# Kernel tuning notes

Hardware: AMD Instinct MI355X
Metric: run time of the kernel (lower is better)

The kernel has to match this reference:

```python
import jax, jax.numpy as jnp
import numpy as np

N_NODES = 100000
N_EDGES = 1600000
DIMS = [21, 32, 64, 128, 21]  # conv1..conv4 (conv4 in-dim fixed to 128; source's 100 is a bug)


def _glorot(key, fan_in, fan_out):
    s = jnp.sqrt(6.0 / (fan_in + fan_out))
    return jax.random.uniform(key, (fan_in, fan_out), jnp.float32, -s, s)


def setup_inputs() -> dict:
    key = jax.random.key(0)
    ks = jax.random.split(key, 6)
    x = jax.random.normal(ks[0], (N_NODES, DIMS[0]), jnp.float32)
    edge_index = jax.random.randint(ks[1], (2, N_EDGES), 0, N_NODES, jnp.int64)
    inp = {"x": x, "edge_index": edge_index}
    wkeys = jax.random.split(ks[2], 4)
    for i in range(4):
        inp[f"W{i+1}"] = _glorot(wkeys[i], DIMS[i], DIMS[i + 1])
        inp[f"b{i+1}"] = jnp.zeros((DIMS[i + 1],), jnp.float32)
    return inp


def gcn_conv(x, row, col, W, b):
    # PyG GCNConv: h = x W; symmetric normalization with self loops; aggregate; + bias
    N = x.shape[0]
    h = x @ W  # [N, F]
    deg = jnp.zeros((N,), h.dtype).at[col].add(1.0) + 1.0  # +1 for self loop
    dinv = jax.lax.rsqrt(deg)
    norm = dinv[row] * dinv[col]  # [E]
    agg = jnp.zeros_like(h).at[col].add(norm[:, None] * h[row])  # scatter messages
    agg = agg + (dinv * dinv)[:, None] * h  # self-loop contribution
    return agg + b


def reference(x, edge_index, W1, b1, W2, b2, W3, b3, W4, b4):
    row, col = edge_index[0], edge_index[1]
    x = jax.nn.relu(gcn_conv(x, row, col, W1, b1))
    x = jax.nn.relu(gcn_conv(x, row, col, W2, b2))
    x = jax.nn.relu(gcn_conv(x, row, col, W3, b3))
    x = gcn_conv(x, row, col, W4, b4)
    return x
```

## Files before the change

kernel.cpp:

```cpp
#include <hip/hip_runtime.h>

#define NN 100000
#define NE 1600000
#define SH 7
#define NB_BKT 782
#define BCAP 3072
#define CSRCAP 3200
#define CHUNK 8192
#define TILES_TOTAL 3125
#define PIPE_BLOCKS 512

static inline int cdiv(long long a, int b) { return (int)((a + b - 1) / b); }

__global__ void partition_kernel(const int* __restrict__ row, const int* __restrict__ col,
                                 int* __restrict__ bcur,
                                 unsigned int* __restrict__ packed, int E) {
    __shared__ int lh[NB_BKT];
    __shared__ int lbase[NB_BKT];
    for (int i = threadIdx.x; i < NB_BKT; i += 256) lh[i] = 0;
    __syncthreads();
    int base = blockIdx.x * CHUNK;
    int end = min(base + CHUNK, E);
    for (int e = base + threadIdx.x; e < end; e += 256) atomicAdd(&lh[col[e] >> SH], 1);
    __syncthreads();
    for (int i = threadIdx.x; i < NB_BKT; i += 256) {
        int v = lh[i];
        lbase[i] = v ? atomicAdd(&bcur[i], v) : 0;
        lh[i] = 0;
    }
    __syncthreads();
    for (int e = base + threadIdx.x; e < end; e += 256) {
        int c = col[e];
        int r = row[e];
        int b = c >> SH;
        int off = atomicAdd(&lh[b], 1);
        packed[lbase[b] + off] = ((unsigned)r << 7) | (unsigned)(c & 127);
    }
}

__global__ void bucket_nodes_place(const unsigned int* __restrict__ packed,
                                   const int* __restrict__ bcur, int* __restrict__ rowptr,
                                   int* __restrict__ rowend, float* __restrict__ dinv,
                                   int* __restrict__ csr_row, int N) {
    int b = blockIdx.x;
    __shared__ int lcnt[128];
    __shared__ int lcur[128];
    __shared__ int wt4[4];
    int t = threadIdx.x;
    if (t < 128) lcnt[t] = 0;
    __syncthreads();
    int s = b * BCAP;
    int e = bcur[b];
    for (int i = s + t; i < e; i += 256)
        atomicAdd(&lcnt[packed[i] & 127u], 1);
    __syncthreads();
    int node = (b << SH) + t;
    int v = (t < 128 && node < N) ? lcnt[t] + 1 : 0;
    int lane = t & 63, w = t >> 6;
    int incl = v;
#pragma unroll
    for (int off = 1; off < 64; off <<= 1) {
        int u = __shfl_up(incl, off, 64);
        if (lane >= off) incl += u;
    }
    if (lane == 63) wt4[w] = incl;
    __syncthreads();
    int woff = 0;
    for (int i = 0; i < w; i++) woff += wt4[i];
    int excl = woff + incl - v;
    if (t < 128 && node < N) {
        int start = b * CSRCAP + excl;
        rowptr[node] = start;
        rowend[node] = start + v;
        csr_row[start] = node;
        dinv[node] = rsqrtf((float)v);
        lcur[t] = start + 1;
    }
    __syncthreads();
    for (int i = s + t; i < e; i += 256) {
        unsigned p = packed[i];
        int r = (int)(p >> 7);
        int pos = atomicAdd(&lcur[p & 127u], 1);
        csr_row[pos] = r;
    }
}

__global__ void padx_kernel(const float* __restrict__ x, float* __restrict__ xp,
                            int* __restrict__ bcur, int N) {
    int idx = blockIdx.x * blockDim.x + threadIdx.x;
    if (idx < NB_BKT) bcur[idx] = idx * BCAP;
    if (idx >= N * 32) return;
    int n = idx >> 5;
    int k = idx & 31;
    xp[idx] = (k < 21) ? x[n * 21 + k] : 0.f;
}

template <int LPN, int FIN, int FOUT, int RJ, int OSTRIDE>
__global__ __launch_bounds__(512) void gather_gemm(
    const float4* __restrict__ h, const int* __restrict__ rowptr,
    const int* __restrict__ rowend, const int* __restrict__ csr_row,
    const float* __restrict__ dinv, const float* __restrict__ W,
    const float* __restrict__ b, float* __restrict__ out, int N) {
    constexpr int NT = 512 / LPN;
    constexpr int FINP = 4 * LPN;
    constexpr int XLD = FINP + 1;
    constexpr int JG = FOUT / RJ;
    __shared__ float xs[NT * XLD];
    __shared__ float Ws[FIN * FOUT];
    __shared__ float bs[FOUT];
    const int t = threadIdx.x;

    for (int i = t; i < FIN * FOUT; i += 512) Ws[i] = W[i];
    if (t < FOUT) bs[t] = b[t];

    const int l = t % LPN;
    const int ny = t / LPN;
    const int node = blockIdx.x * NT + ny;
    float4 acc = make_float4(0.f, 0.f, 0.f, 0.f);
    if (node < N) {
        int s = rowptr[node], e = rowend[node];
        float dn = dinv[node];
        int i = s;
        for (; i + 3 < e; i += 4) {
            int r0 = csr_row[i], r1 = csr_row[i + 1], r2 = csr_row[i + 2], r3 = csr_row[i + 3];
            float w0 = dinv[r0] * dn, w1 = dinv[r1] * dn, w2 = dinv[r2] * dn, w3 = dinv[r3] * dn;
            float4 a0 = h[(size_t)r0 * LPN + l];
            float4 a1 = h[(size_t)r1 * LPN + l];
            float4 a2 = h[(size_t)r2 * LPN + l];
            float4 a3 = h[(size_t)r3 * LPN + l];
            acc.x = fmaf(w0, a0.x, acc.x); acc.y = fmaf(w0, a0.y, acc.y);
            acc.z = fmaf(w0, a0.z, acc.z); acc.w = fmaf(w0, a0.w, acc.w);
            acc.x = fmaf(w1, a1.x, acc.x); acc.y = fmaf(w1, a1.y, acc.y);
            acc.z = fmaf(w1, a1.z, acc.z); acc.w = fmaf(w1, a1.w, acc.w);
            acc.x = fmaf(w2, a2.x, acc.x); acc.y = fmaf(w2, a2.y, acc.y);
            acc.z = fmaf(w2, a2.z, acc.z); acc.w = fmaf(w2, a2.w, acc.w);
            acc.x = fmaf(w3, a3.x, acc.x); acc.y = fmaf(w3, a3.y, acc.y);
            acc.z = fmaf(w3, a3.z, acc.z); acc.w = fmaf(w3, a3.w, acc.w);
        }
        for (; i < e; i++) {
            int r0 = csr_row[i];
            float w0 = dinv[r0] * dn;
            float4 a0 = h[(size_t)r0 * LPN + l];
            acc.x = fmaf(w0, a0.x, acc.x); acc.y = fmaf(w0, a0.y, acc.y);
            acc.z = fmaf(w0, a0.z, acc.z); acc.w = fmaf(w0, a0.w, acc.w);
        }
    }
    xs[ny * XLD + 4 * l + 0] = acc.x;
    xs[ny * XLD + 4 * l + 1] = acc.y;
    xs[ny * XLD + 4 * l + 2] = acc.z;
    xs[ny * XLD + 4 * l + 3] = acc.w;
    __syncthreads();

    const int jg = t % JG;
    const int ng = t / JG;
    float r[RJ];
#pragma unroll
    for (int jj = 0; jj < RJ; jj++) r[jj] = 0.f;
#pragma unroll 4
    for (int k = 0; k < FIN; k++) {
        float xv = xs[ng * XLD + k];
#pragma unroll
        for (int jj = 0; jj < RJ; jj++)
            r[jj] = fmaf(xv, Ws[k * FOUT + jg * RJ + jj], r[jj]);
    }
    int onode = blockIdx.x * NT + ng;
    if (onode < N) {
        float* orow = out + (size_t)onode * OSTRIDE + jg * RJ;
#pragma unroll
        for (int jj = 0; jj < RJ; jj++) r[jj] = fmaxf(r[jj] + bs[jg * RJ + jj], 0.f);
#pragma unroll
        for (int c = 0; c < RJ / 4; c++)
            *(float4*)&orow[4 * c] = make_float4(r[4 * c], r[4 * c + 1], r[4 * c + 2], r[4 * c + 3]);
    }
}

template <int LPN, bool BIAS, bool STORE21>
__global__ void gather4_kernel(const float4* __restrict__ h, const int* __restrict__ rowptr,
                               const int* __restrict__ rowend, const int* __restrict__ csr_row,
                               const float* __restrict__ dinv, const float* __restrict__ bias,
                               float* __restrict__ outp, int N) {
    int node = blockIdx.x * blockDim.y + threadIdx.y;
    if (node >= N) return;
    int l = threadIdx.x;
    int s = rowptr[node], e = rowend[node];
    float dn = dinv[node];
    float4 acc = make_float4(0.f, 0.f, 0.f, 0.f);
    int i = s;
    for (; i + 3 < e; i += 4) {
        int r0 = csr_row[i], r1 = csr_row[i + 1], r2 = csr_row[i + 2], r3 = csr_row[i + 3];
        float w0 = dinv[r0] * dn, w1 = dinv[r1] * dn, w2 = dinv[r2] * dn, w3 = dinv[r3] * dn;
        float4 a0 = h[(size_t)r0 * LPN + l];
        float4 a1 = h[(size_t)r1 * LPN + l];
        float4 a2 = h[(size_t)r2 * LPN + l];
        float4 a3 = h[(size_t)r3 * LPN + l];
        acc.x = fmaf(w0, a0.x, acc.x); acc.y = fmaf(w0, a0.y, acc.y);
        acc.z = fmaf(w0, a0.z, acc.z); acc.w = fmaf(w0, a0.w, acc.w);
        acc.x = fmaf(w1, a1.x, acc.x); acc.y = fmaf(w1, a1.y, acc.y);
        acc.z = fmaf(w1, a1.z, acc.z); acc.w = fmaf(w1, a1.w, acc.w);
        acc.x = fmaf(w2, a2.x, acc.x); acc.y = fmaf(w2, a2.y, acc.y);
        acc.z = fmaf(w2, a2.z, acc.z); acc.w = fmaf(w2, a2.w, acc.w);
        acc.x = fmaf(w3, a3.x, acc.x); acc.y = fmaf(w3, a3.y, acc.y);
        acc.z = fmaf(w3, a3.z, acc.z); acc.w = fmaf(w3, a3.w, acc.w);
    }
    for (; i < e; i++) {
        int r0 = csr_row[i];
        float w0 = dinv[r0] * dn;
        float4 a0 = h[(size_t)r0 * LPN + l];
        acc.x = fmaf(w0, a0.x, acc.x); acc.y = fmaf(w0, a0.y, acc.y);
        acc.z = fmaf(w0, a0.z, acc.z); acc.w = fmaf(w0, a0.w, acc.w);
    }
    if (STORE21) {
        int j = 4 * l;
        float v[4] = {acc.x, acc.y, acc.z, acc.w};
#pragma unroll
        for (int c = 0; c < 4; c++) {
            int jj = j + c;
            if (jj < 21) outp[(size_t)node * 21 + jj] = v[c] + (BIAS ? bias[jj] : 0.f);
        }
    } else {
        ((float4*)outp)[(size_t)node * LPN + l] = acc;
    }
}

__global__ __launch_bounds__(512, 4) void gather_gemm_l3l4_pipe(
    const float4* __restrict__ h, const int* __restrict__ rowptr,
    const int* __restrict__ rowend, const int* __restrict__ csr_row,
    const float* __restrict__ dinv, const float* __restrict__ W3,
    const float* __restrict__ b3, const float* __restrict__ W4,
    float* __restrict__ out, int N) {
    __shared__ float xs[2][32 * 65];
    __shared__ float4 W3v[64 * 32];
    __shared__ float4 W4v[16 * 48];
    __shared__ float b3s[128];
    const int t = threadIdx.x;
    const int b = blockIdx.x;

    for (int d = t; d < 64 * 32; d += 512) {
        int k = d >> 5;
        int jg = d & 7;
        int c = (d >> 3) & 3;
        W3v[d] = ((const float4*)W3)[(k << 5) + (jg << 2) + c];
    }
    for (int cid = t; cid < 16 * 48; cid += 512) {
        int i = cid / 48, rem = cid - i * 48;
        int jq = rem >> 3, jg = rem & 7;
        int k = jg * 16 + i;
        float v0 = (4 * jq + 0 < 21) ? W4[k * 21 + 4 * jq + 0] : 0.f;
        float v1 = (4 * jq + 1 < 21) ? W4[k * 21 + 4 * jq + 1] : 0.f;
        float v2 = (4 * jq + 2 < 21) ? W4[k * 21 + 4 * jq + 2] : 0.f;
        float v3 = (4 * jq + 3 < 21) ? W4[k * 21 + 4 * jq + 3] : 0.f;
        W4v[cid] = make_float4(v0, v1, v2, v3);
    }
    if (t < 128) b3s[t] = b3[t];
    __syncthreads();

    const int R = (TILES_TOTAL - b + PIPE_BLOCKS - 1) / PIPE_BLOCKS;

    for (int r = 0; r <= R; r++) {
        if (t < 256) {
            if (r < R) {
                const int l = t & 7;
                const int ny = t >> 3;
                const int node = (b + PIPE_BLOCKS * r) * 32 + ny;
                float4 acc0 = make_float4(0.f, 0.f, 0.f, 0.f);
                float4 acc1 = make_float4(0.f, 0.f, 0.f, 0.f);
                if (node < N) {
                    int s = rowptr[node], e = rowend[node];
                    float dn = dinv[node];
                    int i = s;
                    for (; i + 3 < e; i += 4) {
                        int r0 = csr_row[i], r1 = csr_row[i + 1];
                        int r2 = csr_row[i + 2], r3 = csr_row[i + 3];
                        float w0 = dinv[r0] * dn, w1 = dinv[r1] * dn;
                        float w2 = dinv[r2] * dn, w3 = dinv[r3] * dn;
                        const float4* p0 = h + (size_t)r0 * 16 + 2 * l;
                        const float4* p1 = h + (size_t)r1 * 16 + 2 * l;
                        const float4* p2 = h + (size_t)r2 * 16 + 2 * l;
                        const float4* p3 = h + (size_t)r3 * 16 + 2 * l;
                        float4 a0 = p0[0], c0 = p0[1];
                        float4 a1 = p1[0], c1 = p1[1];
                        float4 a2 = p2[0], c2 = p2[1];
                        float4 a3 = p3[0], c3 = p3[1];
                        acc0.x = fmaf(w0, a0.x, acc0.x); acc0.y = fmaf(w0, a0.y, acc0.y);
                        acc0.z = fmaf(w0, a0.z, acc0.z); acc0.w = fmaf(w0, a0.w, acc0.w);
                        acc1.x = fmaf(w0, c0.x, acc1.x); acc1.y = fmaf(w0, c0.y, acc1.y);
                        acc1.z = fmaf(w0, c0.z, acc1.z); acc1.w = fmaf(w0, c0.w, acc1.w);
                        acc0.x = fmaf(w1, a1.x, acc0.x); acc0.y = fmaf(w1, a1.y, acc0.y);
                        acc0.z = fmaf(w1, a1.z, acc0.z); acc0.w = fmaf(w1, a1.w, acc0.w);
                        acc1.x = fmaf(w1, c1.x, acc1.x); acc1.y = fmaf(w1, c1.y, acc1.y);
                        acc1.z = fmaf(w1, c1.z, acc1.z); acc1.w = fmaf(w1, c1.w, acc1.w);
                        acc0.x = fmaf(w2, a2.x, acc0.x); acc0.y = fmaf(w2, a2.y, acc0.y);
                        acc0.z = fmaf(w2, a2.z, acc0.z); acc0.w = fmaf(w2, a2.w, acc0.w);
                        acc1.x = fmaf(w2, c2.x, acc1.x); acc1.y = fmaf(w2, c2.y, acc1.y);
                        acc1.z = fmaf(w2, c2.z, acc1.z); acc1.w = fmaf(w2, c2.w, acc1.w);
                        acc0.x = fmaf(w3, a3.x, acc0.x); acc0.y = fmaf(w3, a3.y, acc0.y);
                        acc0.z = fmaf(w3, a3.z, acc0.z); acc0.w = fmaf(w3, a3.w, acc0.w);
                        acc1.x = fmaf(w3, c3.x, acc1.x); acc1.y = fmaf(w3, c3.y, acc1.y);
                        acc1.z = fmaf(w3, c3.z, acc1.z); acc1.w = fmaf(w3, c3.w, acc1.w);
                    }
                    for (; i < e; i++) {
                        int r0 = csr_row[i];
                        float w0 = dinv[r0] * dn;
                        const float4* p0 = h + (size_t)r0 * 16 + 2 * l;
                        float4 a0 = p0[0], c0 = p0[1];
                        acc0.x = fmaf(w0, a0.x, acc0.x); acc0.y = fmaf(w0, a0.y, acc0.y);
                        acc0.z = fmaf(w0, a0.z, acc0.z); acc0.w = fmaf(w0, a0.w, acc0.w);
                        acc1.x = fmaf(w0, c0.x, acc1.x); acc1.y = fmaf(w0, c0.y, acc1.y);
                        acc1.z = fmaf(w0, c0.z, acc1.z); acc1.w = fmaf(w0, c0.w, acc1.w);
                    }
                }
                float* xr = xs[r & 1] + ny * 65 + 8 * l;
                xr[0] = acc0.x; xr[1] = acc0.y; xr[2] = acc0.z; xr[3] = acc0.w;
                xr[4] = acc1.x; xr[5] = acc1.y; xr[6] = acc1.z; xr[7] = acc1.w;
            }
        } else {
            if (r >= 1) {
                const int jg = t & 7;
                const int ng = (t >> 3) & 31;
                const int node = (b + PIPE_BLOCKS * (r - 1)) * 32 + ng;
                const float* arow = xs[(r - 1) & 1] + ng * 65;

                float accA[16];
#pragma unroll
                for (int jj = 0; jj < 16; jj++) accA[jj] = 0.f;
#pragma unroll 4
                for (int k = 0; k < 64; k++) {
                    float xa = arow[k];
                    const float4* wb = &W3v[(k << 5) + jg];
#pragma unroll
                    for (int c = 0; c < 4; c++) {
                        float4 w = wb[c << 3];
                        accA[4 * c + 0] = fmaf(xa, w.x, accA[4 * c + 0]);
                        accA[4 * c + 1] = fmaf(xa, w.y, accA[4 * c + 1]);
                        accA[4 * c + 2] = fmaf(xa, w.z, accA[4 * c + 2]);
                        accA[4 * c + 3] = fmaf(xa, w.w, accA[4 * c + 3]);
                    }
                }
#pragma unroll
                for (int jj = 0; jj < 16; jj++) {
                    float bb = b3s[jg * 16 + jj];
                    accA[jj] = fmaxf(accA[jj] + bb, 0.f);
                }

                float pA[24];
#pragma unroll
                for (int j = 0; j < 24; j++) pA[j] = 0.f;
#pragma unroll
                for (int i = 0; i < 16; i++) {
                    float ha = accA[i];
                    const float4* wb = &W4v[i * 48 + jg];
#pragma unroll
                    for (int jq = 0; jq < 6; jq++) {
                        float4 w = wb[jq << 3];
                        pA[4 * jq + 0] = fmaf(ha, w.x, pA[4 * jq + 0]);
                        pA[4 * jq + 1] = fmaf(ha, w.y, pA[4 * jq + 1]);
                        pA[4 * jq + 2] = fmaf(ha, w.z, pA[4 * jq + 2]);
                        pA[4 * jq + 3] = fmaf(ha, w.w, pA[4 * jq + 3]);
                    }
                }
#pragma unroll
                for (int m = 1; m < 8; m <<= 1) {
#pragma unroll
                    for (int j = 0; j < 24; j++)
                        pA[j] += __shfl_xor(pA[j], m, 8);
                }
                if (node < N) {
                    float* orow = out + (size_t)node * 32 + jg * 3;
                    orow[0] = pA[jg * 3 + 0];
                    orow[1] = pA[jg * 3 + 1];
                    orow[2] = pA[jg * 3 + 2];
                    if (jg < 2) *(float4*)(out + (size_t)node * 32 + 24 + 4 * jg) =
                        make_float4(0.f, 0.f, 0.f, 0.f);
                }
            }
        }
        __syncthreads();
    }
}

extern "C" void kernel_launch(void* const* d_in, const int* in_sizes, int n_in,
                              void* d_out, int out_size, void* d_ws, size_t ws_size,
                              hipStream_t stream) {
    const float* x  = (const float*)d_in[0];
    const int*   ei = (const int*)d_in[1];
    const float* W1 = (const float*)d_in[2]; const float* b1 = (const float*)d_in[3];
    const float* W2 = (const float*)d_in[4]; const float* b2 = (const float*)d_in[5];
    const float* W3 = (const float*)d_in[6]; const float* b3 = (const float*)d_in[7];
    const float* W4 = (const float*)d_in[8]; const float* b4 = (const float*)d_in[9];
    const int* row = ei;
    const int* col = ei + NE;
    float* out = (float*)d_out;

    float* A      = (float*)d_ws;
    float* B      = A + (size_t)NN * 128;
    float* dinv   = B + (size_t)NN * 128;
    int*   rowptr = (int*)(dinv + NN);
    int*   rowend = rowptr + NN;
    int*   csr_row= rowend + NN;
    int*   bcur   = csr_row + (size_t)NB_BKT * CSRCAP;
    unsigned int* packed = (unsigned int*)A;

    const int BS = 256;
    const int NCH = cdiv(NE, CHUNK);

    padx_kernel<<<cdiv((long long)NN * 32, BS), BS, 0, stream>>>(x, B, bcur, NN);
    partition_kernel<<<NCH, 256, 0, stream>>>(row, col, bcur, packed, NE);
    bucket_nodes_place<<<NB_BKT, 256, 0, stream>>>(packed, bcur, rowptr, rowend, dinv, csr_row, NN);

    gather_gemm<8, 21, 32, 4, 32><<<cdiv(NN, 64), 512, 0, stream>>>(
        (const float4*)B, rowptr, rowend, csr_row, dinv, W1, b1, A, NN);
    gather_gemm<8, 32, 64, 8, 64><<<cdiv(NN, 64), 512, 0, stream>>>(
        (const float4*)A, rowptr, rowend, csr_row, dinv, W2, b2, B, NN);
    gather_gemm_l3l4_pipe<<<PIPE_BLOCKS, 512, 0, stream>>>(
        (const float4*)B, rowptr, rowend, csr_row, dinv, W3, b3, W4, A, NN);
    {
        dim3 blk(8, 32);
        gather4_kernel<8, true, true><<<cdiv(NN, 32), blk, 0, stream>>>(
            (const float4*)A, rowptr, rowend, csr_row, dinv, b4, out, NN);
    }
}
```

Before: 312.7 us.

## Use atomic tile counter for dynamic scheduling in fused layer3/4 pipeline kernel

Replaces the static round-robin tile assignment in the fused layer-3/layer-4 producer/consumer kernel with a global atomic tile counter. The counter is reset in padx_kernel and prefetched into a small shared ring, which is meant to balance the uneven per-tile gather cost across blocks. The gather loop gains an 8-way unrolled path for more loads in flight. The consumer half now computes two nodes per thread with 16 threads per node pair, reusing each W3/W4 shared load across both nodes, and the shared tile is padded to 68 floats per row so float4 stores and loads stay aligned. This adds atomic traffic and more register pressure per consumer thread.

```diff
diff --git a/kernel.cpp b/kernel.cpp
--- a/kernel.cpp
+++ b/kernel.cpp
@@ -86,8 +86,9 @@
 }
 
 __global__ void padx_kernel(const float* __restrict__ x, float* __restrict__ xp,
-                            int* __restrict__ bcur, int N) {
+                            int* __restrict__ bcur, int* __restrict__ tctr, int N) {
     int idx = blockIdx.x * blockDim.x + threadIdx.x;
+    if (idx == 0) *tctr = 0;
     if (idx < NB_BKT) bcur[idx] = idx * BCAP;
     if (idx >= N * 32) return;
     int n = idx >> 5;
@@ -222,18 +223,19 @@
     }
 }
 
+#define XLD3 68
 __global__ __launch_bounds__(512, 4) void gather_gemm_l3l4_pipe(
     const float4* __restrict__ h, const int* __restrict__ rowptr,
     const int* __restrict__ rowend, const int* __restrict__ csr_row,
     const float* __restrict__ dinv, const float* __restrict__ W3,
     const float* __restrict__ b3, const float* __restrict__ W4,
-    float* __restrict__ out, int N) {
-    __shared__ float xs[2][32 * 65];
+    int* __restrict__ tctr, float* __restrict__ out, int N) {
+    __shared__ float xs[2][32 * XLD3];
     __shared__ float4 W3v[64 * 32];
     __shared__ float4 W4v[16 * 48];
     __shared__ float b3s[128];
+    __shared__ int tid4[4];
     const int t = threadIdx.x;
-    const int b = blockIdx.x;
 
     for (int d = t; d < 64 * 32; d += 512) {
         int k = d >> 5;
@@ -252,103 +254,144 @@
         W4v[cid] = make_float4(v0, v1, v2, v3);
     }
     if (t < 128) b3s[t] = b3[t];
-    __syncthreads();
-
-    const int R = (TILES_TOTAL - b + PIPE_BLOCKS - 1) / PIPE_BLOCKS;
-
-    for (int r = 0; r <= R; r++) {
+    if (t == 0) tid4[0] = atomicAdd(tctr, 1);
+    __syncthreads();
+
+    for (int r = 0;; r++) {
+        const int tprod = tid4[r & 3];
+        const int tcons = (r > 0) ? tid4[(r - 1) & 3] : TILES_TOTAL;
+        if (t == 0)
+            tid4[(r + 1) & 3] = (tprod < TILES_TOTAL) ? atomicAdd(tctr, 1) : TILES_TOTAL;
+
         if (t < 256) {
-            if (r < R) {
+            if (tprod < TILES_TOTAL) {
                 const int l = t & 7;
                 const int ny = t >> 3;
-                const int node = (b + PIPE_BLOCKS * r) * 32 + ny;
+                const int node = tprod * 32 + ny;
                 float4 acc0 = make_float4(0.f, 0.f, 0.f, 0.f);
                 float4 acc1 = make_float4(0.f, 0.f, 0.f, 0.f);
-                if (node < N) {
-                    int s = rowptr[node], e = rowend[node];
-                    float dn = dinv[node];
-                    int i = s;
-                    for (; i + 3 < e; i += 4) {
-                        int r0 = csr_row[i], r1 = csr_row[i + 1];
-                        int r2 = csr_row[i + 2], r3 = csr_row[i + 3];
-                        float w0 = dinv[r0] * dn, w1 = dinv[r1] * dn;
-                        float w2 = dinv[r2] * dn, w3 = dinv[r3] * dn;
-                        const float4* p0 = h + (size_t)r0 * 16 + 2 * l;
-                        const float4* p1 = h + (size_t)r1 * 16 + 2 * l;
-                        const float4* p2 = h + (size_t)r2 * 16 + 2 * l;
-                        const float4* p3 = h + (size_t)r3 * 16 + 2 * l;
-                        float4 a0 = p0[0], c0 = p0[1];
-                        float4 a1 = p1[0], c1 = p1[1];
-                        float4 a2 = p2[0], c2 = p2[1];
-                        float4 a3 = p3[0], c3 = p3[1];
-                        acc0.x = fmaf(w0, a0.x, acc0.x); acc0.y = fmaf(w0, a0.y, acc0.y);
-                        acc0.z = fmaf(w0, a0.z, acc0.z); acc0.w = fmaf(w0, a0.w, acc0.w);
-                        acc1.x = fmaf(w0, c0.x, acc1.x); acc1.y = fmaf(w0, c0.y, acc1.y);
-                        acc1.z = fmaf(w0, c0.z, acc1.z); acc1.w = fmaf(w0, c0.w, acc1.w);
-                        acc0.x = fmaf(w1, a1.x, acc0.x); acc0.y = fmaf(w1, a1.y, acc0.y);
-                        acc0.z = fmaf(w1, a1.z, acc0.z); acc0.w = fmaf(w1, a1.w, acc0.w);
-                        acc1.x = fmaf(w1, c1.x, acc1.x); acc1.y = fmaf(w1, c1.y, acc1.y);
-                        acc1.z = fmaf(w1, c1.z, acc1.z); acc1.w = fmaf(w1, c1.w, acc1.w);
-                        acc0.x = fmaf(w2, a2.x, acc0.x); acc0.y = fmaf(w2, a2.y, acc0.y);
-                        acc0.z = fmaf(w2, a2.z, acc0.z); acc0.w = fmaf(w2, a2.w, acc0.w);
-                        acc1.x = fmaf(w2, c2.x, acc1.x); acc1.y = fmaf(w2, c2.y, acc1.y);
-                        acc1.z = fmaf(w2, c2.z, acc1.z); acc1.w = fmaf(w2, c2.w, acc1.w);
-                        acc0.x = fmaf(w3, a3.x, acc0.x); acc0.y = fmaf(w3, a3.y, acc0.y);
-                        acc0.z = fmaf(w3, a3.z, acc0.z); acc0.w = fmaf(w3, a3.w, acc0.w);
-                        acc1.x = fmaf(w3, c3.x, acc1.x); acc1.y = fmaf(w3, c3.y, acc1.y);
-                        acc1.z = fmaf(w3, c3.z, acc1.z); acc1.w = fmaf(w3, c3.w, acc1.w);
-                    }
-                    for (; i < e; i++) {
-                        int r0 = csr_row[i];
-                        float w0 = dinv[r0] * dn;
-                        const float4* p0 = h + (size_t)r0 * 16 + 2 * l;
-                        float4 a0 = p0[0], c0 = p0[1];
-                        acc0.x = fmaf(w0, a0.x, acc0.x); acc0.y = fmaf(w0, a0.y, acc0.y);
-                        acc0.z = fmaf(w0, a0.z, acc0.z); acc0.w = fmaf(w0, a0.w, acc0.w);
-                        acc1.x = fmaf(w0, c0.x, acc1.x); acc1.y = fmaf(w0, c0.y, acc1.y);
-                        acc1.z = fmaf(w0, c0.z, acc1.z); acc1.w = fmaf(w0, c0.w, acc1.w);
-                    }
-                }
-                float* xr = xs[r & 1] + ny * 65 + 8 * l;
-                xr[0] = acc0.x; xr[1] = acc0.y; xr[2] = acc0.z; xr[3] = acc0.w;
-                xr[4] = acc1.x; xr[5] = acc1.y; xr[6] = acc1.z; xr[7] = acc1.w;
+                int s = rowptr[node], e = rowend[node];
+                float dn = dinv[node];
+                int i = s;
+                for (; i + 7 < e; i += 8) {
+                    int rr[8];
+                    float ww[8];
+#pragma unroll
+                    for (int u = 0; u < 8; u++) rr[u] = csr_row[i + u];
+#pragma unroll
+                    for (int u = 0; u < 8; u++) ww[u] = dinv[rr[u]] * dn;
+                    float4 a[8], c[8];
+#pragma unroll
+                    for (int u = 0; u < 8; u++) {
+                        const float4* p = h + (size_t)rr[u] * 16 + 2 * l;
+                        a[u] = p[0];
+                        c[u] = p[1];
+                    }
+#pragma unroll
+                    for (int u = 0; u < 8; u++) {
+                        acc0.x = fmaf(ww[u], a[u].x, acc0.x);
+                        acc0.y = fmaf(ww[u], a[u].y, acc0.y);
+                        acc0.z = fmaf(ww[u], a[u].z, acc0.z);
+                        acc0.w = fmaf(ww[u], a[u].w, acc0.w);
+                        acc1.x = fmaf(ww[u], c[u].x, acc1.x);
+                        acc1.y = fmaf(ww[u], c[u].y, acc1.y);
+                        acc1.z = fmaf(ww[u], c[u].z, acc1.z);
+                        acc1.w = fmaf(ww[u], c[u].w, acc1.w);
+                    }
+                }
+                for (; i + 3 < e; i += 4) {
+                    int r0 = csr_row[i], r1 = csr_row[i + 1];
+                    int r2 = csr_row[i + 2], r3 = csr_row[i + 3];
+                    float w0 = dinv[r0] * dn, w1 = dinv[r1] * dn;
+                    float w2 = dinv[r2] * dn, w3 = dinv[r3] * dn;
+                    const float4* p0 = h + (size_t)r0 * 16 + 2 * l;
+                    const float4* p1 = h + (size_t)r1 * 16 + 2 * l;
+                    const float4* p2 = h + (size_t)r2 * 16 + 2 * l;
+                    const float4* p3 = h + (size_t)r3 * 16 + 2 * l;
+                    float4 a0 = p0[0], c0 = p0[1];
+                    float4 a1 = p1[0], c1 = p1[1];
+                    float4 a2 = p2[0], c2 = p2[1];
+                    float4 a3 = p3[0], c3 = p3[1];
+                    acc0.x = fmaf(w0, a0.x, acc0.x); acc0.y = fmaf(w0, a0.y, acc0.y);
+                    acc0.z = fmaf(w0, a0.z, acc0.z); acc0.w = fmaf(w0, a0.w, acc0.w);
+                    acc1.x = fmaf(w0, c0.x, acc1.x); acc1.y = fmaf(w0, c0.y, acc1.y);
+                    acc1.z = fmaf(w0, c0.z, acc1.z); acc1.w = fmaf(w0, c0.w, acc1.w);
+                    acc0.x = fmaf(w1, a1.x, acc0.x); acc0.y = fmaf(w1, a1.y, acc0.y);
+                    acc0.z = fmaf(w1, a1.z, acc0.z); acc0.w = fmaf(w1, a1.w, acc0.w);
+                    acc1.x = fmaf(w1, c1.x, acc1.x); acc1.y = fmaf(w1, c1.y, acc1.y);
+                    acc1.z = fmaf(w1, c1.z, acc1.z); acc1.w = fmaf(w1, c1.w, acc1.w);
+                    acc0.x = fmaf(w2, a2.x, acc0.x); acc0.y = fmaf(w2, a2.y, acc0.y);
+                    acc0.z = fmaf(w2, a2.z, acc0.z); acc0.w = fmaf(w2, a2.w, acc0.w);
+                    acc1.x = fmaf(w2, c2.x, acc1.x); acc1.y = fmaf(w2, c2.y, acc1.y);
+                    acc1.z = fmaf(w2, c2.z, acc1.z); acc1.w = fmaf(w2, c2.w, acc1.w);
+                    acc0.x = fmaf(w3, a3.x, acc0.x); acc0.y = fmaf(w3, a3.y, acc0.y);
+                    acc0.z = fmaf(w3, a3.z, acc0.z); acc0.w = fmaf(w3, a3.w, acc0.w);
+                    acc1.x = fmaf(w3, c3.x, acc1.x); acc1.y = fmaf(w3, c3.y, acc1.y);
+                    acc1.z = fmaf(w3, c3.z, acc1.z); acc1.w = fmaf(w3, c3.w, acc1.w);
+                }
+                for (; i < e; i++) {
+                    int r0 = csr_row[i];
+                    float w0 = dinv[r0] * dn;
+                    const float4* p0 = h + (size_t)r0 * 16 + 2 * l;
+                    float4 a0 = p0[0], c0 = p0[1];
+                    acc0.x = fmaf(w0, a0.x, acc0.x); acc0.y = fmaf(w0, a0.y, acc0.y);
+                    acc0.z = fmaf(w0, a0.z, acc0.z); acc0.w = fmaf(w0, a0.w, acc0.w);
+                    acc1.x = fmaf(w0, c0.x, acc1.x); acc1.y = fmaf(w0, c0.y, acc1.y);
+                    acc1.z = fmaf(w0, c0.z, acc1.z); acc1.w = fmaf(w0, c0.w, acc1.w);
+                }
+                float* xr = xs[r & 1] + ny * XLD3 + 8 * l;
+                *(float4*)(xr + 0) = acc0;
+                *(float4*)(xr + 4) = acc1;
             }
         } else {
-            if (r >= 1) {
-                const int jg = t & 7;
-                const int ng = (t >> 3) & 31;
-                const int node = (b + PIPE_BLOCKS * (r - 1)) * 32 + ng;
-                const float* arow = xs[(r - 1) & 1] + ng * 65;
-
-                float accA[16];
-#pragma unroll
-                for (int jj = 0; jj < 16; jj++) accA[jj] = 0.f;
-#pragma unroll 4
-                for (int k = 0; k < 64; k++) {
-                    float xa = arow[k];
-                    const float4* wb = &W3v[(k << 5) + jg];
-#pragma unroll
-                    for (int c = 0; c < 4; c++) {
-                        float4 w = wb[c << 3];
-                        accA[4 * c + 0] = fmaf(xa, w.x, accA[4 * c + 0]);
-                        accA[4 * c + 1] = fmaf(xa, w.y, accA[4 * c + 1]);
-                        accA[4 * c + 2] = fmaf(xa, w.z, accA[4 * c + 2]);
-                        accA[4 * c + 3] = fmaf(xa, w.w, accA[4 * c + 3]);
-                    }
-                }
-#pragma unroll
-                for (int jj = 0; jj < 16; jj++) {
-                    float bb = b3s[jg * 16 + jj];
+            if (r > 0 && tcons < TILES_TOTAL) {
+                const int tc = t - 256;
+                const int jg16 = tc & 15;
+                const int pr = tc >> 4;
+                const int n0 = tcons * 32 + 2 * pr;
+                const float* arow0 = xs[(r - 1) & 1] + (2 * pr) * XLD3;
+                const float* arow1 = arow0 + XLD3;
+                const int wbase = ((jg16 & 1) << 4) + (jg16 >> 1);
+
+                float accA[8], accB[8];
+#pragma unroll
+                for (int jj = 0; jj < 8; jj++) { accA[jj] = 0.f; accB[jj] = 0.f; }
+                for (int k4 = 0; k4 < 64; k4 += 4) {
+                    float4 x0 = *(const float4*)(arow0 + k4);
+                    float4 x1 = *(const float4*)(arow1 + k4);
+                    float xv0[4] = {x0.x, x0.y, x0.z, x0.w};
+                    float xv1[4] = {x1.x, x1.y, x1.z, x1.w};
+#pragma unroll
+                    for (int kk = 0; kk < 4; kk++) {
+                        float4 w0 = W3v[((k4 + kk) << 5) + wbase];
+                        float4 w1 = W3v[((k4 + kk) << 5) + wbase + 8];
+                        float xa = xv0[kk];
+                        float xb = xv1[kk];
+                        accA[0] = fmaf(xa, w0.x, accA[0]); accA[1] = fmaf(xa, w0.y, accA[1]);
+                        accA[2] = fmaf(xa, w0.z, accA[2]); accA[3] = fmaf(xa, w0.w, accA[3]);
+                        accA[4] = fmaf(xa, w1.x, accA[4]); accA[5] = fmaf(xa, w1.y, accA[5]);
+                        accA[6] = fmaf(xa, w1.z, accA[6]); accA[7] = fmaf(xa, w1.w, accA[7]);
+                        accB[0] = fmaf(xb, w0.x, accB[0]); accB[1] = fmaf(xb, w0.y, accB[1]);
+                        accB[2] = fmaf(xb, w0.z, accB[2]); accB[3] = fmaf(xb, w0.w, accB[3]);
+                        accB[4] = fmaf(xb, w1.x, accB[4]); accB[5] = fmaf(xb, w1.y, accB[5]);
+                        accB[6] = fmaf(xb, w1.z, accB[6]); accB[7] = fmaf(xb, w1.w, accB[7]);
+                    }
+                }
+#pragma unroll
+                for (int jj = 0; jj < 8; jj++) {
+                    float bb = b3s[jg16 * 8 + jj];
                     accA[jj] = fmaxf(accA[jj] + bb, 0.f);
-                }
-
-                float pA[24];
-#pragma unroll
-                for (int j = 0; j < 24; j++) pA[j] = 0.f;
-#pragma unroll
-                for (int i = 0; i < 16; i++) {
-                    float ha = accA[i];
-                    const float4* wb = &W4v[i * 48 + jg];
+                    accB[jj] = fmaxf(accB[jj] + bb, 0.f);
+                }
+
+                float pA[24], pB[24];
+#pragma unroll
+                for (int j = 0; j < 24; j++) { pA[j] = 0.f; pB[j] = 0.f; }
+#pragma unroll
+                for (int jj = 0; jj < 8; jj++) {
+                    float ha = accA[jj];
+                    float hb = accB[jj];
+                    const float4* wb = &W4v[(((jg16 & 1) << 3) + jj) * 48 + (jg16 >> 1)];
 #pragma unroll
                     for (int jq = 0; jq < 6; jq++) {
                         float4 w = wb[jq << 3];
@@ -356,25 +399,40 @@
                         pA[4 * jq + 1] = fmaf(ha, w.y, pA[4 * jq + 1]);
                         pA[4 * jq + 2] = fmaf(ha, w.z, pA[4 * jq + 2]);
                         pA[4 * jq + 3] = fmaf(ha, w.w, pA[4 * jq + 3]);
-                    }
-                }
-#pragma unroll
-                for (int m = 1; m < 8; m <<= 1) {
-#pragma unroll
-                    for (int j = 0; j < 24; j++)
-                        pA[j] += __shfl_xor(pA[j], m, 8);
-                }
-                if (node < N) {
-                    float* orow = out + (size_t)node * 32 + jg * 3;
-                    orow[0] = pA[jg * 3 + 0];
-                    orow[1] = pA[jg * 3 + 1];
-                    orow[2] = pA[jg * 3 + 2];
-                    if (jg < 2) *(float4*)(out + (size_t)node * 32 + 24 + 4 * jg) =
-                        make_float4(0.f, 0.f, 0.f, 0.f);
+                        pB[4 * jq + 0] = fmaf(hb, w.x, pB[4 * jq + 0]);
+                        pB[4 * jq + 1] = fmaf(hb, w.y, pB[4 * jq + 1]);
+                        pB[4 * jq + 2] = fmaf(hb, w.z, pB[4 * jq + 2]);
+                        pB[4 * jq + 3] = fmaf(hb, w.w, pB[4 * jq + 3]);
+                    }
+                }
+#pragma unroll
+                for (int m = 1; m < 16; m <<= 1) {
+#pragma unroll
+                    for (int j = 0; j < 24; j++) {
+                        pA[j] += __shfl_xor(pA[j], m, 16);
+                        pB[j] += __shfl_xor(pB[j], m, 16);
+                    }
+                }
+                if (jg16 < 8) {
+                    float* orowA = out + (size_t)n0 * 32 + jg16 * 3;
+                    orowA[0] = pA[jg16 * 3 + 0];
+                    orowA[1] = pA[jg16 * 3 + 1];
+                    orowA[2] = pA[jg16 * 3 + 2];
+                    float* orowB = out + (size_t)(n0 + 1) * 32 + jg16 * 3;
+                    orowB[0] = pB[jg16 * 3 + 0];
+                    orowB[1] = pB[jg16 * 3 + 1];
+                    orowB[2] = pB[jg16 * 3 + 2];
+                    if (jg16 < 2) {
+                        *(float4*)(out + (size_t)n0 * 32 + 24 + 4 * jg16) =
+                            make_float4(0.f, 0.f, 0.f, 0.f);
+                        *(float4*)(out + (size_t)(n0 + 1) * 32 + 24 + 4 * jg16) =
+                            make_float4(0.f, 0.f, 0.f, 0.f);
+                    }
                 }
             }
         }
         __syncthreads();
+        if (r > 0 && tcons >= TILES_TOTAL) break;
     }
 }
 
@@ -398,12 +456,13 @@
     int*   rowend = rowptr + NN;
     int*   csr_row= rowend + NN;
     int*   bcur   = csr_row + (size_t)NB_BKT * CSRCAP;
+    int*   tctr   = bcur + NB_BKT;
     unsigned int* packed = (unsigned int*)A;
 
     const int BS = 256;
     const int NCH = cdiv(NE, CHUNK);
 
-    padx_kernel<<<cdiv((long long)NN * 32, BS), BS, 0, stream>>>(x, B, bcur, NN);
+    padx_kernel<<<cdiv((long long)NN * 32, BS), BS, 0, stream>>>(x, B, bcur, tctr, NN);
     partition_kernel<<<NCH, 256, 0, stream>>>(row, col, bcur, packed, NE);
     bucket_nodes_place<<<NB_BKT, 256, 0, stream>>>(packed, bcur, rowptr, rowend, dinv, csr_row, NN);
 
@@ -412,7 +471,7 @@
     gather_gemm<8, 32, 64, 8, 64><<<cdiv(NN, 64), 512, 0, stream>>>(
         (const float4*)A, rowptr, rowend, csr_row, dinv, W2, b2, B, NN);
     gather_gemm_l3l4_pipe<<<PIPE_BLOCKS, 512, 0, stream>>>(
-        (const float4*)B, rowptr, rowend, csr_row, dinv, W3, b3, W4, A, NN);
+        (const float4*)B, rowptr, rowend, csr_row, dinv, W3, b3, W4, tctr, A, NN);
     {
         dim3 blk(8, 32);
         gather4_kernel<8, true, true><<<cdiv(NN, 32), blk, 0, stream>>>(
```

Measured after the change: 347.1 us. +11.0%, slower.

## Use dynamic tile scheduling and 64-node tiles in fused layer3/4 pipeline

Applied to the files above, without the earlier changes.

The fused layer-3/layer-4 pipelined kernel now takes tiles from a global atomic counter instead of a static round-robin assignment. Tiles grow to 64 nodes, with each gather thread holding 16 features, and each GEMM consumer thread computes two nodes so every W3/W4 shared-memory load is reused twice. Shared tiles use an XOR swizzle with float4 accesses instead of padding, and the layer-4 reduction is reorganised so each lane writes a float4. This aims to reduce load imbalance from irregular degrees and to cut shared-memory traffic, at the cost of more registers, a global atomic per tile, and an extra counter reset in padx.

```diff
diff --git a/kernel.cpp b/kernel.cpp
--- a/kernel.cpp
+++ b/kernel.cpp
@@ -7,7 +7,7 @@
 #define BCAP 3072
 #define CSRCAP 3200
 #define CHUNK 8192
-#define TILES_TOTAL 3125
+#define NTILES 1563
 #define PIPE_BLOCKS 512
 
 static inline int cdiv(long long a, int b) { return (int)((a + b - 1) / b); }
@@ -86,8 +86,9 @@
 }
 
 __global__ void padx_kernel(const float* __restrict__ x, float* __restrict__ xp,
-                            int* __restrict__ bcur, int N) {
+                            int* __restrict__ bcur, int* __restrict__ tctr, int N) {
     int idx = blockIdx.x * blockDim.x + threadIdx.x;
+    if (idx == 0) *tctr = 0;
     if (idx < NB_BKT) bcur[idx] = idx * BCAP;
     if (idx >= N * 32) return;
     int n = idx >> 5;
@@ -222,18 +223,20 @@
     }
 }
 
-__global__ __launch_bounds__(512, 4) void gather_gemm_l3l4_pipe(
+__global__ __launch_bounds__(512)
+__attribute__((amdgpu_waves_per_eu(4, 4)))
+void gather_gemm_l3l4_pipe(
     const float4* __restrict__ h, const int* __restrict__ rowptr,
     const int* __restrict__ rowend, const int* __restrict__ csr_row,
     const float* __restrict__ dinv, const float* __restrict__ W3,
     const float* __restrict__ b3, const float* __restrict__ W4,
-    float* __restrict__ out, int N) {
-    __shared__ float xs[2][32 * 65];
+    int* __restrict__ tctr, float* __restrict__ out, int N) {
+    __shared__ float xs[2][64 * 64];
     __shared__ float4 W3v[64 * 32];
     __shared__ float4 W4v[16 * 48];
     __shared__ float b3s[128];
+    __shared__ int tid4[4];
     const int t = threadIdx.x;
-    const int b = blockIdx.x;
 
     for (int d = t; d < 64 * 32; d += 512) {
         int k = d >> 5;
@@ -252,129 +255,156 @@
         W4v[cid] = make_float4(v0, v1, v2, v3);
     }
     if (t < 128) b3s[t] = b3[t];
-    __syncthreads();
-
-    const int R = (TILES_TOTAL - b + PIPE_BLOCKS - 1) / PIPE_BLOCKS;
-
-    for (int r = 0; r <= R; r++) {
+    if (t == 0) tid4[0] = atomicAdd(tctr, 1);
+    __syncthreads();
+
+    for (int r = 0;; r++) {
+        const int tprod = tid4[r & 3];
+        const int tcons = (r > 0) ? tid4[(r - 1) & 3] : NTILES;
+        if (t == 0)
+            tid4[(r + 1) & 3] = (tprod < NTILES) ? atomicAdd(tctr, 1) : NTILES;
+
         if (t < 256) {
-            if (r < R) {
-                const int l = t & 7;
-                const int ny = t >> 3;
-                const int node = (b + PIPE_BLOCKS * r) * 32 + ny;
+            if (tprod < NTILES) {
+                const int l = t & 3;
+                const int ny = t >> 2;
+                const int node = tprod * 64 + ny;
                 float4 acc0 = make_float4(0.f, 0.f, 0.f, 0.f);
                 float4 acc1 = make_float4(0.f, 0.f, 0.f, 0.f);
+                float4 acc2 = make_float4(0.f, 0.f, 0.f, 0.f);
+                float4 acc3 = make_float4(0.f, 0.f, 0.f, 0.f);
                 if (node < N) {
                     int s = rowptr[node], e = rowend[node];
                     float dn = dinv[node];
                     int i = s;
-                    for (; i + 3 < e; i += 4) {
+                    for (; i + 1 < e; i += 2) {
                         int r0 = csr_row[i], r1 = csr_row[i + 1];
-                        int r2 = csr_row[i + 2], r3 = csr_row[i + 3];
                         float w0 = dinv[r0] * dn, w1 = dinv[r1] * dn;
-                        float w2 = dinv[r2] * dn, w3 = dinv[r3] * dn;
-                        const float4* p0 = h + (size_t)r0 * 16 + 2 * l;
-                        const float4* p1 = h + (size_t)r1 * 16 + 2 * l;
-                        const float4* p2 = h + (size_t)r2 * 16 + 2 * l;
-                        const float4* p3 = h + (size_t)r3 * 16 + 2 * l;
-                        float4 a0 = p0[0], c0 = p0[1];
-                        float4 a1 = p1[0], c1 = p1[1];
-                        float4 a2 = p2[0], c2 = p2[1];
-                        float4 a3 = p3[0], c3 = p3[1];
+                        const float4* p0 = h + (size_t)r0 * 16 + 4 * l;
+                        const float4* p1 = h + (size_t)r1 * 16 + 4 * l;
+                        float4 a0 = p0[0], a1 = p0[1], a2 = p0[2], a3 = p0[3];
+                        float4 b0 = p1[0], b1 = p1[1], b2 = p1[2], b3_ = p1[3];
                         acc0.x = fmaf(w0, a0.x, acc0.x); acc0.y = fmaf(w0, a0.y, acc0.y);
                         acc0.z = fmaf(w0, a0.z, acc0.z); acc0.w = fmaf(w0, a0.w, acc0.w);
-                        acc1.x = fmaf(w0, c0.x, acc1.x); acc1.y = fmaf(w0, c0.y, acc1.y);
-                        acc1.z = fmaf(w0, c0.z, acc1.z); acc1.w = fmaf(w0, c0.w, acc1.w);
-                        acc0.x = fmaf(w1, a1.x, acc0.x); acc0.y = fmaf(w1, a1.y, acc0.y);
-                        acc0.z = fmaf(w1, a1.z, acc0.z); acc0.w = fmaf(w1, a1.w, acc0.w);
-                        acc1.x = fmaf(w1, c1.x, acc1.x); acc1.y = fmaf(w1, c1.y, acc1.y);
-                        acc1.z = fmaf(w1, c1.z, acc1.z); acc1.w = fmaf(w1, c1.w, acc1.w);
-                        acc0.x = fmaf(w2, a2.x, acc0.x); acc0.y = fmaf(w2, a2.y, acc0.y);
-                        acc0.z = fmaf(w2, a2.z, acc0.z); acc0.w = fmaf(w2, a2.w, acc0.w);
-                        acc1.x = fmaf(w2, c2.x, acc1.x); acc1.y = fmaf(w2, c2.y, acc1.y);
-                        acc1.z = fmaf(w2, c2.z, acc1.z); acc1.w = fmaf(w2, c2.w, acc1.w);
-                        acc0.x = fmaf(w3, a3.x, acc0.x); acc0.y = fmaf(w3, a3.y, acc0.y);
-                        acc0.z = fmaf(w3, a3.z, acc0.z); acc0.w = fmaf(w3, a3.w, acc0.w);
-                        acc1.x = fmaf(w3, c3.x, acc1.x); acc1.y = fmaf(w3, c3.y, acc1.y);
-                        acc1.z = fmaf(w3, c3.z, acc1.z); acc1.w = fmaf(w3, c3.w, acc1.w);
-                    }
-                    for (; i < e; i++) {
+                        acc1.x = fmaf(w0, a1.x, acc1.x); acc1.y = fmaf(w0, a1.y, acc1.y);
+                        acc1.z = fmaf(w0, a1.z, acc1.z); acc1.w = fmaf(w0, a1.w, acc1.w);
+                        acc2.x = fmaf(w0, a2.x, acc2.x); acc2.y = fmaf(w0, a2.y, acc2.y);
+                        acc2.z = fmaf(w0, a2.z, acc2.z); acc2.w = fmaf(w0, a2.w, acc2.w);
+                        acc3.x = fmaf(w0, a3.x, acc3.x); acc3.y = fmaf(w0, a3.y, acc3.y);
+                        acc3.z = fmaf(w0, a3.z, acc3.z); acc3.w = fmaf(w0, a3.w, acc3.w);
+                        acc0.x = fmaf(w1, b0.x, acc0.x); acc0.y = fmaf(w1, b0.y, acc0.y);
+                        acc0.z = fmaf(w1, b0.z, acc0.z); acc0.w = fmaf(w1, b0.w, acc0.w);
+                        acc1.x = fmaf(w1, b1.x, acc1.x); acc1.y = fmaf(w1, b1.y, acc1.y);
+                        acc1.z = fmaf(w1, b1.z, acc1.z); acc1.w = fmaf(w1, b1.w, acc1.w);
+                        acc2.x = fmaf(w1, b2.x, acc2.x); acc2.y = fmaf(w1, b2.y, acc2.y);
+                        acc2.z = fmaf(w1, b2.z, acc2.z); acc2.w = fmaf(w1, b2.w, acc2.w);
+                        acc3.x = fmaf(w1, b3_.x, acc3.x); acc3.y = fmaf(w1, b3_.y, acc3.y);
+                        acc3.z = fmaf(w1, b3_.z, acc3.z); acc3.w = fmaf(w1, b3_.w, acc3.w);
+                    }
+                    if (i < e) {
                         int r0 = csr_row[i];
                         float w0 = dinv[r0] * dn;
-                        const float4* p0 = h + (size_t)r0 * 16 + 2 * l;
-                        float4 a0 = p0[0], c0 = p0[1];
+                        const float4* p0 = h + (size_t)r0 * 16 + 4 * l;
+                        float4 a0 = p0[0], a1 = p0[1], a2 = p0[2], a3 = p0[3];
                         acc0.x = fmaf(w0, a0.x, acc0.x); acc0.y = fmaf(w0, a0.y, acc0.y);
                         acc0.z = fmaf(w0, a0.z, acc0.z); acc0.w = fmaf(w0, a0.w, acc0.w);
-                        acc1.x = fmaf(w0, c0.x, acc1.x); acc1.y = fmaf(w0, c0.y, acc1.y);
-                        acc1.z = fmaf(w0, c0.z, acc1.z); acc1.w = fmaf(w0, c0.w, acc1.w);
+                        acc1.x = fmaf(w0, a1.x, acc1.x); acc1.y = fmaf(w0, a1.y, acc1.y);
+                        acc1.z = fmaf(w0, a1.z, acc1.z); acc1.w = fmaf(w0, a1.w, acc1.w);
+                        acc2.x = fmaf(w0, a2.x, acc2.x); acc2.y = fmaf(w0, a2.y, acc2.y);
+                        acc2.z = fmaf(w0, a2.z, acc2.z); acc2.w = fmaf(w0, a2.w, acc2.w);
+                        acc3.x = fmaf(w0, a3.x, acc3.x); acc3.y = fmaf(w0, a3.y, acc3.y);
+                        acc3.z = fmaf(w0, a3.z, acc3.z); acc3.w = fmaf(w0, a3.w, acc3.w);
                     }
                 }
-                float* xr = xs[r & 1] + ny * 65 + 8 * l;
-                xr[0] = acc0.x; xr[1] = acc0.y; xr[2] = acc0.z; xr[3] = acc0.w;
-                xr[4] = acc1.x; xr[5] = acc1.y; xr[6] = acc1.z; xr[7] = acc1.w;
+                float* xw = xs[r & 1] + ny * 64;
+                const int sw = (ny >> 1) & 7;
+                *(float4*)(xw + 4 * ((4 * l + 0) ^ sw)) = acc0;
+                *(float4*)(xw + 4 * ((4 * l + 1) ^ sw)) = acc1;
+                *(float4*)(xw + 4 * ((4 * l + 2) ^ sw)) = acc2;
+                *(float4*)(xw + 4 * ((4 * l + 3) ^ sw)) = acc3;
             }
         } else {
-            if (r >= 1) {
-                const int jg = t & 7;
-                const int ng = (t >> 3) & 31;
-                const int node = (b + PIPE_BLOCKS * (r - 1)) * 32 + ng;
-                const float* arow = xs[(r - 1) & 1] + ng * 65;
-
-                float accA[16];
-#pragma unroll
-                for (int jj = 0; jj < 16; jj++) accA[jj] = 0.f;
-#pragma unroll 4
-                for (int k = 0; k < 64; k++) {
-                    float xa = arow[k];
-                    const float4* wb = &W3v[(k << 5) + jg];
-#pragma unroll
-                    for (int c = 0; c < 4; c++) {
-                        float4 w = wb[c << 3];
-                        accA[4 * c + 0] = fmaf(xa, w.x, accA[4 * c + 0]);
-                        accA[4 * c + 1] = fmaf(xa, w.y, accA[4 * c + 1]);
-                        accA[4 * c + 2] = fmaf(xa, w.z, accA[4 * c + 2]);
-                        accA[4 * c + 3] = fmaf(xa, w.w, accA[4 * c + 3]);
+            if (r > 0 && tcons < NTILES) {
+                const int tc = t - 256;
+                const int jg = tc & 7;
+                const int pp = tc >> 3;
+                const int nA = tcons * 64 + 2 * pp;
+                const float* xsrd = xs[(r - 1) & 1] + (2 * pp) * 64;
+                const int sw = pp & 7;
+
+                float accA[16], accB[16];
+#pragma unroll
+                for (int jj = 0; jj < 16; jj++) { accA[jj] = 0.f; accB[jj] = 0.f; }
+#pragma unroll 2
+                for (int k4 = 0; k4 < 64; k4 += 4) {
+                    const int f = (k4 >> 2) ^ sw;
+                    float4 xA = *(const float4*)(xsrd + 4 * f);
+                    float4 xB = *(const float4*)(xsrd + 64 + 4 * f);
+                    float xva[4] = {xA.x, xA.y, xA.z, xA.w};
+                    float xvb[4] = {xB.x, xB.y, xB.z, xB.w};
+#pragma unroll
+                    for (int kk = 0; kk < 4; kk++) {
+                        const int k = k4 + kk;
+#pragma unroll
+                        for (int c = 0; c < 4; c++) {
+                            float4 w = W3v[(k << 5) + (c << 3) + jg];
+                            accA[4 * c + 0] = fmaf(xva[kk], w.x, accA[4 * c + 0]);
+                            accA[4 * c + 1] = fmaf(xva[kk], w.y, accA[4 * c + 1]);
+                            accA[4 * c + 2] = fmaf(xva[kk], w.z, accA[4 * c + 2]);
+                            accA[4 * c + 3] = fmaf(xva[kk], w.w, accA[4 * c + 3]);
+                            accB[4 * c + 0] = fmaf(xvb[kk], w.x, accB[4 * c + 0]);
+                            accB[4 * c + 1] = fmaf(xvb[kk], w.y, accB[4 * c + 1]);
+                            accB[4 * c + 2] = fmaf(xvb[kk], w.z, accB[4 * c + 2]);
+                            accB[4 * c + 3] = fmaf(xvb[kk], w.w, accB[4 * c + 3]);
+                        }
                     }
                 }
 #pragma unroll
                 for (int jj = 0; jj < 16; jj++) {
                     float bb = b3s[jg * 16 + jj];
                     accA[jj] = fmaxf(accA[jj] + bb, 0.f);
+                    accB[jj] = fmaxf(accB[jj] + bb, 0.f);
                 }
 
-                float pA[24];
-#pragma unroll
-                for (int j = 0; j < 24; j++) pA[j] = 0.f;
-#pragma unroll
-                for (int i = 0; i < 16; i++) {
-                    float ha = accA[i];
-                    const float4* wb = &W4v[i * 48 + jg];
-#pragma unroll
-                    for (int jq = 0; jq < 6; jq++) {
-                        float4 w = wb[jq << 3];
-                        pA[4 * jq + 0] = fmaf(ha, w.x, pA[4 * jq + 0]);
-                        pA[4 * jq + 1] = fmaf(ha, w.y, pA[4 * jq + 1]);
-                        pA[4 * jq + 2] = fmaf(ha, w.z, pA[4 * jq + 2]);
-                        pA[4 * jq + 3] = fmaf(ha, w.w, pA[4 * jq + 3]);
+                float sA[4] = {0.f, 0.f, 0.f, 0.f};
+                float sB[4] = {0.f, 0.f, 0.f, 0.f};
+#pragma unroll
+                for (int jq = 0; jq < 6; jq++) {
+                    float pqA[4] = {0.f, 0.f, 0.f, 0.f};
+                    float pqB[4] = {0.f, 0.f, 0.f, 0.f};
+#pragma unroll
+                    for (int i = 0; i < 16; i++) {
+                        float4 w = W4v[i * 48 + (jq << 3) + jg];
+                        float ha = accA[i];
+                        float hb = accB[i];
+                        pqA[0] = fmaf(ha, w.x, pqA[0]); pqA[1] = fmaf(ha, w.y, pqA[1]);
+                        pqA[2] = fmaf(ha, w.z, pqA[2]); pqA[3] = fmaf(ha, w.w, pqA[3]);
+                        pqB[0] = fmaf(hb, w.x, pqB[0]); pqB[1] = fmaf(hb, w.y, pqB[1]);
+                        pqB[2] = fmaf(hb, w.z, pqB[2]); pqB[3] = fmaf(hb, w.w, pqB[3]);
+                    }
+#pragma unroll
+                    for (int m = 1; m < 8; m <<= 1) {
+#pragma unroll
+                        for (int j = 0; j < 4; j++) {
+                            pqA[j] += __shfl_xor(pqA[j], m, 8);
+                            pqB[j] += __shfl_xor(pqB[j], m, 8);
+                        }
+                    }
+                    if (jg == jq) {
+                        sA[0] = pqA[0]; sA[1] = pqA[1]; sA[2] = pqA[2]; sA[3] = pqA[3];
+                        sB[0] = pqB[0]; sB[1] = pqB[1]; sB[2] = pqB[2]; sB[3] = pqB[3];
                     }
                 }
-#pragma unroll
-                for (int m = 1; m < 8; m <<= 1) {
-#pragma unroll
-                    for (int j = 0; j < 24; j++)
-                        pA[j] += __shfl_xor(pA[j], m, 8);
-                }
-                if (node < N) {
-                    float* orow = out + (size_t)node * 32 + jg * 3;
-                    orow[0] = pA[jg * 3 + 0];
-                    orow[1] = pA[jg * 3 + 1];
-                    orow[2] = pA[jg * 3 + 2];
-                    if (jg < 2) *(float4*)(out + (size_t)node * 32 + 24 + 4 * jg) =
-                        make_float4(0.f, 0.f, 0.f, 0.f);
+                if (nA < N) {
+                    float4 vA = make_float4(sA[0], sA[1], sA[2], sA[3]);
+                    float4 vB = make_float4(sB[0], sB[1], sB[2], sB[3]);
+                    *(float4*)(out + (size_t)nA * 32 + 4 * jg) = vA;
+                    *(float4*)(out + (size_t)(nA + 1) * 32 + 4 * jg) = vB;
                 }
             }
         }
         __syncthreads();
+        if (r > 0 && tcons >= NTILES) break;
     }
 }
 
@@ -398,12 +428,13 @@
     int*   rowend = rowptr + NN;
     int*   csr_row= rowend + NN;
     int*   bcur   = csr_row + (size_t)NB_BKT * CSRCAP;
+    int*   tctr   = bcur + NB_BKT;
     unsigned int* packed = (unsigned int*)A;
 
     const int BS = 256;
     const int NCH = cdiv(NE, CHUNK);
 
-    padx_kernel<<<cdiv((long long)NN * 32, BS), BS, 0, stream>>>(x, B, bcur, NN);
+    padx_kernel<<<cdiv((long long)NN * 32, BS), BS, 0, stream>>>(x, B, bcur, tctr, NN);
     partition_kernel<<<NCH, 256, 0, stream>>>(row, col, bcur, packed, NE);
     bucket_nodes_place<<<NB_BKT, 256, 0, stream>>>(packed, bcur, rowptr, rowend, dinv, csr_row, NN);
 
@@ -412,7 +443,7 @@
     gather_gemm<8, 32, 64, 8, 64><<<cdiv(NN, 64), 512, 0, stream>>>(
         (const float4*)A, rowptr, rowend, csr_row, dinv, W2, b2, B, NN);
     gather_gemm_l3l4_pipe<<<PIPE_BLOCKS, 512, 0, stream>>>(
-        (const float4*)B, rowptr, rowend, csr_row, dinv, W3, b3, W4, A, NN);
+        (const float4*)B, rowptr, rowend, csr_row, dinv, W3, b3, W4, tctr, A, NN);
     {
         dim3 blk(8, 32);
         gather4_kernel<8, true, true><<<cdiv(NN, 32), blk, 0, stream>>>(
```

New measurement: 334.1 us. +6.9%, slower.
